# Kernel tuning notes

Hardware: AMD Instinct MI355X
Metric: run time of the kernel (lower is better)

## Reference

```python
import jax, jax.numpy as jnp
import numpy as np

B, V, NFEAT, INTER, NHID1, NHID12, NCLASS = 131072, 8, 32, 8, 16, 8, 2


def setup_inputs() -> dict:
    key = jax.random.key(0)
    ks = jax.random.split(key, 16)
    # node feature tensor: channel 0 = node type in {0,1}, channels 1..32 = features
    types = jax.random.randint(ks[0], (B, V, 1), 0, 2).astype(jnp.float32)
    feats = jax.random.normal(ks[1], (B, V, NFEAT), dtype=jnp.float32)
    x = jnp.concatenate([types, feats], axis=-1)  # (B, V, 33)
    adj = jax.random.uniform(ks[2], (B, V, V), dtype=jnp.float32)
    edge_attr = jax.random.normal(ks[3], (B, V, V), dtype=jnp.float32)
    s = lambda k, *sh: jax.random.normal(k, sh, dtype=jnp.float32) * 0.1
    return {
        "x": x, "adj": adj, "edge_attr": edge_attr,
        "wa": s(ks[4], INTER, NFEAT), "ba": jnp.zeros((INTER,), jnp.float32),
        "wb": s(ks[5], INTER, NFEAT), "bb": jnp.zeros((INTER,), jnp.float32),
        "w1": s(ks[6], NFEAT, NHID1), "b1": jnp.zeros((NHID1,), jnp.float32),
        "w2": s(ks[7], NHID1, NHID12), "b2": jnp.zeros((NHID12,), jnp.float32),
        "wg": s(ks[8], NHID12, NHID12), "bg": jnp.zeros((NHID12,), jnp.float32),
        "wf": s(ks[9], NCLASS, NHID12), "bf": jnp.zeros((NCLASS,), jnp.float32),
    }


def _attn_pool(h, wg, bg):
    # GlobalAttentionPooling: softmax(gate_nn(h)) over nodes, weighted sum
    gate = jax.nn.softmax(jnp.einsum('bvc,oc->bvo', h, wg) + bg, axis=1)
    return jnp.sum(gate * h, axis=1)  # (B, NHID12)


def reference(x, adj, edge_attr, wa, ba, wb, bb, w1, b1, w2, b2, wg, bg, wf, bf):
    node_types = x[..., 0]           # (B, V)
    feat = x[..., 1:]                # (B, V, 32)
    # conv_b (1x1 conv == per-node linear), output layout (B, inter, V)
    Fk = jnp.einsum('bvc,oc->bov', feat, wb) + bb[None, :, None]  # (B, 8, V=8)
    S = jax.nn.softmax(jnp.matmul(Fk, Fk), axis=1)                # (B, 8, 8)
    W = adj * (S + edge_attr)                                     # (B, V, V)
    # graph conv 1: (W @ feat) @ w1 + b1, LeakyReLU(0.01)
    h = jax.nn.leaky_relu(jnp.einsum('bvw,bwc->bvc', W, feat) @ w1 + b1)
    # graph conv 2
    h = jax.nn.leaky_relu(jnp.einsum('bvw,bwc->bvc', W, h) @ w2 + b2)  # (B, V, 8)
    # per-type masked attention pooling; types fixed to {0, 1}
    pooled = []
    for t in (0.0, 1.0):
        mask = (node_types == t)[..., None].astype(h.dtype)
        pooled.append(_attn_pool(h * mask, wg, bg))
    x_pool = jnp.mean(jnp.stack(pooled, axis=1), axis=1)  # (B, NHID12)
    return x_pool @ wf.T + bf  # (B, NCLASS)
```

## Files before the change

### kernel.cpp

```cpp
#include <hip/hip_runtime.h>


#define SLOTS 32

__device__ __forceinline__ float grp_max(float x) {
    x = fmaxf(x, __shfl_xor(x, 1));
    x = fmaxf(x, __shfl_xor(x, 2));
    x = fmaxf(x, __shfl_xor(x, 4));
    return x;
}
__device__ __forceinline__ float grp_sum(float x) {
    x += __shfl_xor(x, 1);
    x += __shfl_xor(x, 2);
    x += __shfl_xor(x, 4);
    return x;
}

__global__ __launch_bounds__(256, 4)
void gcn_fused(const float* __restrict__ x,
               const float* __restrict__ adj,
               const float* __restrict__ edge,
               const float* __restrict__ wb, const float* __restrict__ bb,
               const float* __restrict__ w1, const float* __restrict__ b1,
               const float* __restrict__ w2, const float* __restrict__ b2,
               const float* __restrict__ wg, const float* __restrict__ bg,
               const float* __restrict__ wf, const float* __restrict__ bf,
               float* __restrict__ out, int Btot)
{
    __shared__ float FkS[SLOTS * 72];
    __shared__ float SS [SLOTS * 72];
    __shared__ float g1S[SLOTS * 136];

    const int tid  = threadIdx.x;
    const int slot = tid >> 3;
    const int v    = tid & 7;
    long long b = (long long)blockIdx.x * SLOTS + slot;
    if (b >= Btot) b = Btot - 1;

    const float* xr = x + (size_t)b * 264 + (size_t)v * 33;
    float xl[33];
#pragma unroll
    for (int i = 0; i < 33; ++i) xl[i] = xr[i];

    const float4* ar = (const float4*)(adj  + (size_t)b * 64 + (size_t)v * 8);
    const float4* er = (const float4*)(edge + (size_t)b * 64 + (size_t)v * 8);
    float4 a0 = ar[0], a1 = ar[1];
    float4 e0 = er[0], e1 = er[1];
    const float type = xl[0];

    float Fk[8];
#pragma unroll
    for (int o = 0; o < 8; ++o) {
        float acc = bb[o];
#pragma unroll
        for (int c = 0; c < 32; ++c) acc += xl[1 + c] * wb[o * 32 + c];
        Fk[o] = acc;
    }

    float g1[16];
#pragma unroll
    for (int j = 0; j < 16; ++j) g1[j] = 0.f;
#pragma unroll
    for (int c = 0; c < 32; ++c) {
        const float f = xl[1 + c];
#pragma unroll
        for (int j = 0; j < 16; ++j) g1[j] += f * w1[c * 16 + j];
    }

#pragma unroll
    for (int o = 0; o < 8; ++o) FkS[slot * 72 + o * 8 + v] = Fk[o];
    {
        float4* gp = (float4*)&g1S[slot * 136 + v * 16];
        gp[0] = make_float4(g1[0],  g1[1],  g1[2],  g1[3]);
        gp[1] = make_float4(g1[4],  g1[5],  g1[6],  g1[7]);
        gp[2] = make_float4(g1[8],  g1[9],  g1[10], g1[11]);
        gp[3] = make_float4(g1[12], g1[13], g1[14], g1[15]);
    }
    __syncthreads();

    float M[8];
#pragma unroll
    for (int o = 0; o < 8; ++o) {
        const float4* fr = (const float4*)&FkS[slot * 72 + o * 8];
        const float4 r0 = fr[0], r1 = fr[1];
        M[o] = r0.x * Fk[0] + r0.y * Fk[1] + r0.z * Fk[2] + r0.w * Fk[3]
             + r1.x * Fk[4] + r1.y * Fk[5] + r1.z * Fk[6] + r1.w * Fk[7];
    }
    float mx = M[0];
#pragma unroll
    for (int o = 1; o < 8; ++o) mx = fmaxf(mx, M[o]);
    float ssum = 0.f;
#pragma unroll
    for (int o = 0; o < 8; ++o) { M[o] = __expf(M[o] - mx); ssum += M[o]; }
    const float sinv = 1.f / ssum;
#pragma unroll
    for (int o = 0; o < 8; ++o) SS[slot * 72 + o * 8 + v] = M[o] * sinv;
    __syncthreads();

    const float4* sr = (const float4*)&SS[slot * 72 + v * 8];
    const float4 s0 = sr[0], s1 = sr[1];
    float W[8];
    W[0] = a0.x * (s0.x + e0.x);  W[1] = a0.y * (s0.y + e0.y);
    W[2] = a0.z * (s0.z + e0.z);  W[3] = a0.w * (s0.w + e0.w);
    W[4] = a1.x * (s1.x + e1.x);  W[5] = a1.y * (s1.y + e1.y);
    W[6] = a1.z * (s1.z + e1.z);  W[7] = a1.w * (s1.w + e1.w);

    float msg1[16];
#pragma unroll
    for (int j = 0; j < 16; ++j) msg1[j] = 0.f;
#pragma unroll
    for (int w = 0; w < 8; ++w) {
        const float wv = W[w];
        const float4* gp = (const float4*)&g1S[slot * 136 + w * 16];
        const float4 q0 = gp[0], q1 = gp[1], q2 = gp[2], q3 = gp[3];
        msg1[0]  += wv * q0.x; msg1[1]  += wv * q0.y; msg1[2]  += wv * q0.z; msg1[3]  += wv * q0.w;
        msg1[4]  += wv * q1.x; msg1[5]  += wv * q1.y; msg1[6]  += wv * q1.z; msg1[7]  += wv * q1.w;
        msg1[8]  += wv * q2.x; msg1[9]  += wv * q2.y; msg1[10] += wv * q2.z; msg1[11] += wv * q2.w;
        msg1[12] += wv * q3.x; msg1[13] += wv * q3.y; msg1[14] += wv * q3.z; msg1[15] += wv * q3.w;
    }
    float h[16];
#pragma unroll
    for (int j = 0; j < 16; ++j) {
        const float t = msg1[j] + b1[j];
        h[j] = t > 0.f ? t : 0.01f * t;
    }

    float g2[8];
#pragma unroll
    for (int n = 0; n < 8; ++n) g2[n] = 0.f;
#pragma unroll
    for (int j = 0; j < 16; ++j) {
        const float hv = h[j];
#pragma unroll
        for (int n = 0; n < 8; ++n) g2[n] += hv * w2[j * 8 + n];
    }
    {
        float4* gp = (float4*)&FkS[slot * 72 + v * 8];
        gp[0] = make_float4(g2[0], g2[1], g2[2], g2[3]);
        gp[1] = make_float4(g2[4], g2[5], g2[6], g2[7]);
    }
    __syncthreads();

    float msg2[8];
#pragma unroll
    for (int n = 0; n < 8; ++n) msg2[n] = 0.f;
#pragma unroll
    for (int w = 0; w < 8; ++w) {
        const float wv = W[w];
        const float4* gp = (const float4*)&FkS[slot * 72 + w * 8];
        const float4 q0 = gp[0], q1 = gp[1];
        msg2[0] += wv * q0.x; msg2[1] += wv * q0.y; msg2[2] += wv * q0.z; msg2[3] += wv * q0.w;
        msg2[4] += wv * q1.x; msg2[5] += wv * q1.y; msg2[6] += wv * q1.z; msg2[7] += wv * q1.w;
    }
    float h2[8];
#pragma unroll
    for (int n = 0; n < 8; ++n) {
        const float t = msg2[n] + b2[n];
        h2[n] = t > 0.f ? t : 0.01f * t;
    }

    float xpool[8];
#pragma unroll
    for (int n = 0; n < 8; ++n) xpool[n] = 0.f;
#pragma unroll
    for (int t = 0; t < 2; ++t) {
        const float tv = (float)t;
        const bool msk = (type == tv);
        float hm[8];
#pragma unroll
        for (int n = 0; n < 8; ++n) hm[n] = msk ? h2[n] : 0.f;
#pragma unroll
        for (int o = 0; o < 8; ++o) {
            float lg = bg[o];
#pragma unroll
            for (int n = 0; n < 8; ++n) lg += hm[n] * wg[o * 8 + n];
            const float m = grp_max(lg);
            const float e = __expf(lg - m);
            const float d = grp_sum(e);
            const float p = grp_sum((e / d) * hm[o]);
            xpool[o] += 0.5f * p;
        }
    }

    if (v < 2) {
        float r = bf[v];
#pragma unroll
        for (int o = 0; o < 8; ++o) r += xpool[o] * wf[v * 8 + o];
        out[(size_t)b * 2 + v] = r;
    }
}

extern "C" void kernel_launch(void* const* d_in, const int* in_sizes, int n_in,
                              void* d_out, int out_size, void* d_ws, size_t ws_size,
                              hipStream_t stream) {
    const float* x    = (const float*)d_in[0];
    const float* adj  = (const float*)d_in[1];
    const float* edge = (const float*)d_in[2];
    const float* wb   = (const float*)d_in[5];
    const float* bb   = (const float*)d_in[6];
    const float* w1   = (const float*)d_in[7];
    const float* b1   = (const float*)d_in[8];
    const float* w2   = (const float*)d_in[9];
    const float* b2   = (const float*)d_in[10];
    const float* wg   = (const float*)d_in[11];
    const float* bg   = (const float*)d_in[12];
    const float* wf   = (const float*)d_in[13];
    const float* bf   = (const float*)d_in[14];
    float* out = (float*)d_out;

    const int Btot = in_sizes[0] / 264;
    const int grid = (Btot + SLOTS - 1) / SLOTS;

    gcn_fused<<<grid, 256, 0, stream>>>(x, adj, edge, wb, bb, w1, b1, w2, b2,
                                        wg, bg, wf, bf, out, Btot);
}
```

Baseline: 303.8 us.

## Restructure attention pooling via LDS transpose and shrink blocks with shared buffer reuse

The masked attention pooling is reorganised so each thread owns one gate channel and loops over the 8 nodes read back from LDS. This replaces the per-channel shuffle max and sum reductions, and removes the gate bias, which cancels in the softmax over nodes. Blocks shrink to 128 threads with 16 graphs each. The three LDS buffers collapse into two reused buffers, protected by extra barriers. The 33-float register copy of x is dropped in favour of streamed loads, which merges the Fk and g1 loops and aims to cut register pressure and raise occupancy.

```diff
diff --git a/kernel.cpp b/kernel.cpp
--- a/kernel.cpp
+++ b/kernel.cpp
@@ -1,22 +1,17 @@
 #include <hip/hip_runtime.h>
 
 
-#define SLOTS 32
-
-__device__ __forceinline__ float grp_max(float x) {
-    x = fmaxf(x, __shfl_xor(x, 1));
-    x = fmaxf(x, __shfl_xor(x, 2));
-    x = fmaxf(x, __shfl_xor(x, 4));
-    return x;
-}
-__device__ __forceinline__ float grp_sum(float x) {
+#define SLOTS 16
+#define NTHREADS 128
+
+__device__ __forceinline__ float grp_sum8(float x) {
     x += __shfl_xor(x, 1);
     x += __shfl_xor(x, 2);
     x += __shfl_xor(x, 4);
     return x;
 }
 
-__global__ __launch_bounds__(256, 4)
+__global__ __launch_bounds__(NTHREADS, 6)
 void gcn_fused(const float* __restrict__ x,
                const float* __restrict__ adj,
                const float* __restrict__ edge,
@@ -27,50 +22,46 @@
                const float* __restrict__ wf, const float* __restrict__ bf,
                float* __restrict__ out, int Btot)
 {
-    __shared__ float FkS[SLOTS * 72];
-    __shared__ float SS [SLOTS * 72];
-    __shared__ float g1S[SLOTS * 136];
+    __shared__ float bufA[SLOTS * 72];
+    __shared__ float bufB[SLOTS * 136];
 
     const int tid  = threadIdx.x;
     const int slot = tid >> 3;
     const int v    = tid & 7;
-    long long b = (long long)blockIdx.x * SLOTS + slot;
-    if (b >= Btot) b = Btot - 1;
-
-    const float* xr = x + (size_t)b * 264 + (size_t)v * 33;
-    float xl[33];
-#pragma unroll
-    for (int i = 0; i < 33; ++i) xl[i] = xr[i];
-
-    const float4* ar = (const float4*)(adj  + (size_t)b * 64 + (size_t)v * 8);
-    const float4* er = (const float4*)(edge + (size_t)b * 64 + (size_t)v * 8);
-    float4 a0 = ar[0], a1 = ar[1];
-    float4 e0 = er[0], e1 = er[1];
-    const float type = xl[0];
+    long long bb_ = (long long)blockIdx.x * SLOTS + slot;
+    if (bb_ >= Btot) bb_ = Btot - 1;
+    const size_t b = (size_t)bb_;
+
+    float* A  = &bufA[slot * 72];
+    float* Bg = &bufB[slot * 136];
+
+    const float4* ar = (const float4*)(adj  + b * 64 + (size_t)v * 8);
+    const float4* er = (const float4*)(edge + b * 64 + (size_t)v * 8);
+    const float4 a0 = ar[0], a1 = ar[1];
+    const float4 e0 = er[0], e1 = er[1];
+
+    const float* xr = x + b * 264 + (size_t)v * 33;
+    const float type = xr[0];
 
     float Fk[8];
 #pragma unroll
-    for (int o = 0; o < 8; ++o) {
-        float acc = bb[o];
-#pragma unroll
-        for (int c = 0; c < 32; ++c) acc += xl[1 + c] * wb[o * 32 + c];
-        Fk[o] = acc;
-    }
-
+    for (int o = 0; o < 8; ++o) Fk[o] = bb[o];
     float g1[16];
 #pragma unroll
     for (int j = 0; j < 16; ++j) g1[j] = 0.f;
 #pragma unroll
     for (int c = 0; c < 32; ++c) {
-        const float f = xl[1 + c];
+        const float f = xr[1 + c];
+#pragma unroll
+        for (int o = 0; o < 8; ++o) Fk[o] += f * wb[o * 32 + c];
 #pragma unroll
         for (int j = 0; j < 16; ++j) g1[j] += f * w1[c * 16 + j];
     }
 
 #pragma unroll
-    for (int o = 0; o < 8; ++o) FkS[slot * 72 + o * 8 + v] = Fk[o];
+    for (int o = 0; o < 8; ++o) A[o * 8 + v] = Fk[o];
     {
-        float4* gp = (float4*)&g1S[slot * 136 + v * 16];
+        float4* gp = (float4*)(Bg + v * 16);
         gp[0] = make_float4(g1[0],  g1[1],  g1[2],  g1[3]);
         gp[1] = make_float4(g1[4],  g1[5],  g1[6],  g1[7]);
         gp[2] = make_float4(g1[8],  g1[9],  g1[10], g1[11]);
@@ -81,11 +72,13 @@
     float M[8];
 #pragma unroll
     for (int o = 0; o < 8; ++o) {
-        const float4* fr = (const float4*)&FkS[slot * 72 + o * 8];
+        const float4* fr = (const float4*)(A + o * 8);
         const float4 r0 = fr[0], r1 = fr[1];
         M[o] = r0.x * Fk[0] + r0.y * Fk[1] + r0.z * Fk[2] + r0.w * Fk[3]
              + r1.x * Fk[4] + r1.y * Fk[5] + r1.z * Fk[6] + r1.w * Fk[7];
     }
+    __syncthreads();
+
     float mx = M[0];
 #pragma unroll
     for (int o = 1; o < 8; ++o) mx = fmaxf(mx, M[o]);
@@ -94,10 +87,10 @@
     for (int o = 0; o < 8; ++o) { M[o] = __expf(M[o] - mx); ssum += M[o]; }
     const float sinv = 1.f / ssum;
 #pragma unroll
-    for (int o = 0; o < 8; ++o) SS[slot * 72 + o * 8 + v] = M[o] * sinv;
-    __syncthreads();
-
-    const float4* sr = (const float4*)&SS[slot * 72 + v * 8];
+    for (int o = 0; o < 8; ++o) A[o * 8 + v] = M[o] * sinv;
+    __syncthreads();
+
+    const float4* sr = (const float4*)(A + v * 8);
     const float4 s0 = sr[0], s1 = sr[1];
     float W[8];
     W[0] = a0.x * (s0.x + e0.x);  W[1] = a0.y * (s0.y + e0.y);
@@ -111,7 +104,7 @@
 #pragma unroll
     for (int w = 0; w < 8; ++w) {
         const float wv = W[w];
-        const float4* gp = (const float4*)&g1S[slot * 136 + w * 16];
+        const float4* gp = (const float4*)(Bg + w * 16);
         const float4 q0 = gp[0], q1 = gp[1], q2 = gp[2], q3 = gp[3];
         msg1[0]  += wv * q0.x; msg1[1]  += wv * q0.y; msg1[2]  += wv * q0.z; msg1[3]  += wv * q0.w;
         msg1[4]  += wv * q1.x; msg1[5]  += wv * q1.y; msg1[6]  += wv * q1.z; msg1[7]  += wv * q1.w;
@@ -134,8 +127,9 @@
 #pragma unroll
         for (int n = 0; n < 8; ++n) g2[n] += hv * w2[j * 8 + n];
     }
+    __syncthreads();
     {
-        float4* gp = (float4*)&FkS[slot * 72 + v * 8];
+        float4* gp = (float4*)(A + v * 8);
         gp[0] = make_float4(g2[0], g2[1], g2[2], g2[3]);
         gp[1] = make_float4(g2[4], g2[5], g2[6], g2[7]);
     }
@@ -147,7 +141,7 @@
 #pragma unroll
     for (int w = 0; w < 8; ++w) {
         const float wv = W[w];
-        const float4* gp = (const float4*)&FkS[slot * 72 + w * 8];
+        const float4* gp = (const float4*)(A + w * 8);
         const float4 q0 = gp[0], q1 = gp[1];
         msg2[0] += wv * q0.x; msg2[1] += wv * q0.y; msg2[2] += wv * q0.z; msg2[3] += wv * q0.w;
         msg2[4] += wv * q1.x; msg2[5] += wv * q1.y; msg2[6] += wv * q1.z; msg2[7] += wv * q1.w;
@@ -158,35 +152,51 @@
         const float t = msg2[n] + b2[n];
         h2[n] = t > 0.f ? t : 0.01f * t;
     }
-
-    float xpool[8];
-#pragma unroll
-    for (int n = 0; n < 8; ++n) xpool[n] = 0.f;
+    __syncthreads();
+
+#pragma unroll
+    for (int n = 0; n < 8; ++n) A[v * 9 + n] = h2[n];
+    A[v * 9 + 8] = type;
+    __syncthreads();
+
+    const int o = v;
+    float d[8], ty[8], ho[8];
+#pragma unroll
+    for (int vp = 0; vp < 8; ++vp) {
+        const float* hr = A + vp * 9;
+        float acc = 0.f;
+#pragma unroll
+        for (int n = 0; n < 8; ++n) acc += hr[n] * wg[o * 8 + n];
+        d[vp] = acc;
+        ty[vp] = hr[8];
+        ho[vp] = hr[o];
+    }
+    float xp = 0.f;
 #pragma unroll
     for (int t = 0; t < 2; ++t) {
         const float tv = (float)t;
-        const bool msk = (type == tv);
-        float hm[8];
-#pragma unroll
-        for (int n = 0; n < 8; ++n) hm[n] = msk ? h2[n] : 0.f;
-#pragma unroll
-        for (int o = 0; o < 8; ++o) {
-            float lg = bg[o];
-#pragma unroll
-            for (int n = 0; n < 8; ++n) lg += hm[n] * wg[o * 8 + n];
-            const float m = grp_max(lg);
-            const float e = __expf(lg - m);
-            const float d = grp_sum(e);
-            const float p = grp_sum((e / d) * hm[o]);
-            xpool[o] += 0.5f * p;
+        float l[8];
+        float lmx = -1e30f;
+#pragma unroll
+        for (int vp = 0; vp < 8; ++vp) {
+            l[vp] = (ty[vp] == tv) ? d[vp] : 0.f;
+            lmx = fmaxf(lmx, l[vp]);
         }
-    }
-
-    if (v < 2) {
-        float r = bf[v];
-#pragma unroll
-        for (int o = 0; o < 8; ++o) r += xpool[o] * wf[v * 8 + o];
-        out[(size_t)b * 2 + v] = r;
+        float esum = 0.f, num = 0.f;
+#pragma unroll
+        for (int vp = 0; vp < 8; ++vp) {
+            const float e = __expf(l[vp] - lmx);
+            esum += e;
+            num  += (ty[vp] == tv) ? e * ho[vp] : 0.f;
+        }
+        xp += 0.5f * num / esum;
+    }
+
+    const float y0 = grp_sum8(xp * wf[0 * 8 + o]);
+    const float y1 = grp_sum8(xp * wf[1 * 8 + o]);
+    if (v == 0) {
+        float2* op = (float2*)(out + b * 2);
+        *op = make_float2(y0 + bf[0], y1 + bf[1]);
     }
 }
 
@@ -211,6 +221,6 @@
     const int Btot = in_sizes[0] / 264;
     const int grid = (Btot + SLOTS - 1) / SLOTS;
 
-    gcn_fused<<<grid, 256, 0, stream>>>(x, adj, edge, wb, bb, w1, b1, w2, b2,
-                                        wg, bg, wf, bf, out, Btot);
+    gcn_fused<<<grid, NTHREADS, 0, stream>>>(x, adj, edge, wb, bb, w1, b1,
+                                             w2, b2, wg, bg, wf, bf, out, Btot);
 }
```

Result: slower. 368.6 us (+21.3%).
